# Kernel optimization log

Hardware: AMD Instinct MI355X
Metric: run time of the kernel (lower is better)

Reference implementation:

```python
import jax, jax.numpy as jnp
import numpy as np

B, CIN, COUT, H, W = 8, 256, 256, 64, 64


def setup_inputs() -> dict:
    key = jax.random.key(0)
    k1, k2, k3 = jax.random.split(key, 3)
    x = jax.random.normal(k1, (B, CIN, H, W), dtype=jnp.float32)
    style = jax.random.normal(k2, (B, CIN), dtype=jnp.float32)
    # kaiming_normal_ (fan_in = CIN*3*3, gain = sqrt(2))
    fan_in = CIN * 9
    weight = jax.random.normal(k3, (COUT, CIN, 3, 3), dtype=jnp.float32) * np.sqrt(2.0 / fan_in)
    return {"x": x, "style": style, "weight": weight}


def reference(x, style, weight):
    b, cin, h, w = x.shape
    cout = weight.shape[0]
    # modulate: [B, Cout, Cin, 3, 3]
    mw = style[:, None, :, None, None] * weight[None]
    # demodulate
    sigma = jnp.sqrt(jnp.sum(mw * mw, axis=(2, 3, 4), keepdims=True) + 1e-8)
    dw = mw / sigma
    # per-sample conv via grouped convolution (groups = B)
    x_g = x.reshape(1, b * cin, h, w)
    w_g = dw.reshape(b * cout, cin, 3, 3)
    out = jax.lax.conv_general_dilated(
        x_g, w_g,
        window_strides=(1, 1),
        padding=((1, 1), (1, 1)),
        feature_group_count=b,
        dimension_numbers=("NCHW", "OIHW", "NCHW"),
    )
    return out.reshape(b, cout, h, w)
```

## Files before the change

kernel.cpp:

```cpp
#include <hip/hip_runtime.h>

#define B_ 8
#define CIN_ 256
#define COUT_ 256

typedef short short8_t __attribute__((ext_vector_type(8)));
typedef float float4_t __attribute__((ext_vector_type(4)));

#define DWA_SHORTS   (B_ * 9 * 32 * COUT_ * 8)
#define XPRE_SHORTS  (B_ * 8 * 66 * 66 * 32)

__device__ __forceinline__ unsigned short f2bf(float f) {
    union { float f; unsigned u; } v; v.f = f;
    unsigned u = v.u;
    unsigned r = (u + 0x7fffu + ((u >> 16) & 1u)) >> 16;
    return (unsigned short)r;
}

__global__ __launch_bounds__(256) void k_xpre(const float* __restrict__ x,
                                              unsigned short* __restrict__ xpre) {
    const int h = blockIdx.x, cb = blockIdx.y, b = blockIdx.z;
    const int t = threadIdx.x;
    const int w = t >> 2, g = t & 3;
    const float* xp = x + (((size_t)(b * CIN_ + cb * 32 + g * 8)) * 64 + h) * 64 + w;
    short8_t v;
#pragma unroll
    for (int j = 0; j < 8; ++j) v[j] = (short)f2bf(xp[(size_t)j * 4096]);
    size_t dst = ((((size_t)(b * 8 + cb)) * 66 + (h + 1)) * 66 + (w + 1)) * 32 + (size_t)g * 8;
    *(short8_t*)(xpre + dst) = v;
}

__global__ __launch_bounds__(256) void k_modulate(const float* __restrict__ weight,
                                                  const float* __restrict__ style,
                                                  unsigned short* __restrict__ dwA) {
    const int b = blockIdx.y;
    const int co = blockIdx.x * 8 + (threadIdx.x & 7);
    const int oct = threadIdx.x >> 3;
    const int lane = threadIdx.x & 63, wid = threadIdx.x >> 6;

    float wreg[72];
    const float* wp = weight + (size_t)co * (CIN_ * 9) + oct * 72;
#pragma unroll
    for (int i = 0; i < 18; ++i)
        *(float4*)(wreg + 4 * i) = *(const float4*)(wp + 4 * i);

    float s[8];
#pragma unroll
    for (int j = 0; j < 8; ++j) s[j] = style[b * CIN_ + oct * 8 + j];

    float part = 0.f;
#pragma unroll
    for (int j = 0; j < 8; ++j) {
        float a = 0.f;
#pragma unroll
        for (int t9 = 0; t9 < 9; ++t9) a += wreg[j * 9 + t9] * wreg[j * 9 + t9];
        part += s[j] * s[j] * a;
    }
    part += __shfl_xor(part, 8, 64);
    part += __shfl_xor(part, 16, 64);
    part += __shfl_xor(part, 32, 64);
    __shared__ float red[4][8];
    if ((lane >> 3) == 0) red[wid][lane & 7] = part;
    __syncthreads();
    const int co_l = threadIdx.x & 7;
    const float tot = red[0][co_l] + red[1][co_l] + red[2][co_l] + red[3][co_l];
    const float inv = 1.0f / sqrtf(tot + 1e-8f);

#pragma unroll
    for (int tap = 0; tap < 9; ++tap) {
        short8_t o;
#pragma unroll
        for (int j = 0; j < 8; ++j) o[j] = (short)f2bf(wreg[j * 9 + tap] * s[j] * inv);
        size_t dst = ((((size_t)(b * 9 + tap)) * 32 + oct) * 256 + co) * 8;
        *(short8_t*)(dwA + dst) = o;
    }
}

__global__ __launch_bounds__(256) void k_conv(const unsigned short* __restrict__ xpre,
                                              const unsigned short* __restrict__ dwA,
                                              float* __restrict__ out) {
    __shared__ __align__(16) unsigned short xs[2][4 * 66 * 40];

    const int rowgrp = blockIdx.x;
    const int co_tile = blockIdx.y;
    const int b = blockIdx.z;
    const int tid = threadIdx.x;
    const int lane = tid & 63, wid = tid >> 6;
    const int wave_m = wid >> 1, wave_n = wid & 1;
    const int quad = lane >> 4, l16 = lane & 15;
    const int r0 = rowgrp * 2;
    const int co_base = co_tile * 128 + wave_m * 64;

    float4_t acc[4][4];
#pragma unroll
    for (int mi = 0; mi < 4; ++mi)
#pragma unroll
        for (int ni = 0; ni < 4; ++ni) acc[mi][ni] = (float4_t){0.f, 0.f, 0.f, 0.f};

    short8_t st[5];
    auto load_regs = [&](int cb) {
        const unsigned short* s = xpre + ((size_t)((b * 8 + cb) * 66 + r0)) * 2112;
#pragma unroll
        for (int it = 0; it < 4; ++it)
            st[it] = *(const short8_t*)(s + (size_t)(tid + it * 256) * 8);
        if (tid < 32) st[4] = *(const short8_t*)(s + (size_t)(tid + 1024) * 8);
    };
    auto store_lds = [&](int buf) {
        unsigned short* d = xs[buf];
#pragma unroll
        for (int it = 0; it < 4; ++it) {
            int c = tid + it * 256;
            *(short8_t*)(d + (c >> 2) * 40 + (c & 3) * 8) = st[it];
        }
        if (tid < 32) {
            int c = tid + 1024;
            *(short8_t*)(d + (c >> 2) * 40 + (c & 3) * 8) = st[4];
        }
    };

    load_regs(0);

    for (int cb = 0; cb < 8; ++cb) {
        short8_t aA[4], aB[4];
        {
            const unsigned short* Ab = dwA + ((size_t)(b * 9 + 0) * 32 + cb * 4 + quad) * 2048;
#pragma unroll
            for (int mi = 0; mi < 4; ++mi)
                aA[mi] = *(const short8_t*)(Ab + (co_base + mi * 16 + l16) * 8);
        }
        store_lds(cb & 1);
        __syncthreads();
        if (cb < 7) load_regs(cb + 1);

        const unsigned short* xb = xs[cb & 1];
#pragma unroll
        for (int tap = 0; tap < 9; ++tap) {
            if (tap < 8) {
                const unsigned short* Ab =
                    dwA + ((size_t)(b * 9 + tap + 1) * 32 + cb * 4 + quad) * 2048;
                short8_t* an = (tap & 1) ? aA : aB;
#pragma unroll
                for (int mi = 0; mi < 4; ++mi)
                    an[mi] = *(const short8_t*)(Ab + (co_base + mi * 16 + l16) * 8);
            }
            const int dh = tap / 3, dwc = tap % 3;
            const unsigned short* brow = xb + (wave_n + dh) * 66 * 40;
            short8_t bf[4];
#pragma unroll
            for (int ni = 0; ni < 4; ++ni)
                bf[ni] = *(const short8_t*)(brow + (ni * 16 + l16 + dwc) * 40 + quad * 8);
            const short8_t* ac = (tap & 1) ? aB : aA;
#pragma unroll
            for (int mi = 0; mi < 4; ++mi)
#pragma unroll
                for (int ni = 0; ni < 4; ++ni)
                    acc[mi][ni] = __builtin_amdgcn_mfma_f32_16x16x32_bf16(
                        ac[mi], bf[ni], acc[mi][ni], 0, 0, 0);
        }
    }

    const int orow = r0 + wave_n;
#pragma unroll
    for (int mi = 0; mi < 4; ++mi)
#pragma unroll
        for (int ni = 0; ni < 4; ++ni)
#pragma unroll
            for (int r = 0; r < 4; ++r) {
                int co = co_base + mi * 16 + quad * 4 + r;
                int c = ni * 16 + l16;
                out[(((size_t)b * COUT_ + co) * 64 + orow) * 64 + c] = acc[mi][ni][r];
            }
}

extern "C" void kernel_launch(void* const* d_in, const int* in_sizes, int n_in,
                              void* d_out, int out_size, void* d_ws, size_t ws_size,
                              hipStream_t stream) {
    const float* x = (const float*)d_in[0];
    const float* style = (const float*)d_in[1];
    const float* weight = (const float*)d_in[2];
    float* out = (float*)d_out;

    unsigned short* dwA = (unsigned short*)d_ws;
    unsigned short* xpre = dwA + DWA_SHORTS;

    hipMemsetAsync((void*)xpre, 0, (size_t)XPRE_SHORTS * 2, stream);
    k_xpre<<<dim3(64, 8, B_), 256, 0, stream>>>(x, xpre);
    k_modulate<<<dim3(32, B_), 256, 0, stream>>>(weight, style, dwA);
    k_conv<<<dim3(32, 2, B_), 256, 0, stream>>>(xpre, dwA, out);
}
```

Measured before the change: 142.6 us.

## Drop padding memset, restructure weight modulation, and deepen A-operand prefetch

The input-packing kernel now writes the zero halo itself across 66 rows, so the separate memset launch over the padded buffer is removed. The modulation kernel loads each weight slice once into LDS and handles all batch samples per block, reducing redundant weight reads, but it now writes scalar 2-byte stores. The convolution kernel keeps a 3-deep register ring of weight fragments, prefetching two taps ahead and across channel-block boundaries to hide global load latency, at the cost of more registers.

Result: no change. 141.8 us (-0.6%).

```diff
diff --git a/kernel.cpp b/kernel.cpp
--- a/kernel.cpp
+++ b/kernel.cpp
@@ -19,61 +19,82 @@
 
 __global__ __launch_bounds__(256) void k_xpre(const float* __restrict__ x,
                                               unsigned short* __restrict__ xpre) {
-    const int h = blockIdx.x, cb = blockIdx.y, b = blockIdx.z;
+    const int h_out = blockIdx.x;
+    const int cb = blockIdx.y, b = blockIdx.z;
     const int t = threadIdx.x;
-    const int w = t >> 2, g = t & 3;
-    const float* xp = x + (((size_t)(b * CIN_ + cb * 32 + g * 8)) * 64 + h) * 64 + w;
-    short8_t v;
-#pragma unroll
-    for (int j = 0; j < 8; ++j) v[j] = (short)f2bf(xp[(size_t)j * 4096]);
-    size_t dst = ((((size_t)(b * 8 + cb)) * 66 + (h + 1)) * 66 + (w + 1)) * 32 + (size_t)g * 8;
-    *(short8_t*)(xpre + dst) = v;
+    const int h_in = h_out - 1;
+    unsigned short* dst_row = xpre + (((size_t)(b * 8 + cb) * 66 + h_out)) * 66 * 32;
+#pragma unroll
+    for (int pass = 0; pass < 2; ++pass) {
+        int p = t + pass * 256;
+        if (p >= 264) break;
+        int w_out = p >> 2, g = p & 3;
+        int w_in = w_out - 1;
+        short8_t v = (short8_t){0, 0, 0, 0, 0, 0, 0, 0};
+        if ((unsigned)h_in < 64u && (unsigned)w_in < 64u) {
+            const float* xp = x + (((size_t)(b * CIN_ + cb * 32 + g * 8)) * 64 + h_in) * 64 + w_in;
+#pragma unroll
+            for (int j = 0; j < 8; ++j) v[j] = (short)f2bf(xp[(size_t)j * 4096]);
+        }
+        *(short8_t*)(dst_row + (size_t)w_out * 32 + g * 8) = v;
+    }
 }
 
 __global__ __launch_bounds__(256) void k_modulate(const float* __restrict__ weight,
                                                   const float* __restrict__ style,
                                                   unsigned short* __restrict__ dwA) {
-    const int b = blockIdx.y;
-    const int co = blockIdx.x * 8 + (threadIdx.x & 7);
-    const int oct = threadIdx.x >> 3;
-    const int lane = threadIdx.x & 63, wid = threadIdx.x >> 6;
-
-    float wreg[72];
-    const float* wp = weight + (size_t)co * (CIN_ * 9) + oct * 72;
-#pragma unroll
-    for (int i = 0; i < 18; ++i)
-        *(float4*)(wreg + 4 * i) = *(const float4*)(wp + 4 * i);
-
-    float s[8];
-#pragma unroll
-    for (int j = 0; j < 8; ++j) s[j] = style[b * CIN_ + oct * 8 + j];
-
-    float part = 0.f;
-#pragma unroll
-    for (int j = 0; j < 8; ++j) {
+    __shared__ float wlds[4 * 2304];
+    const int t = threadIdx.x;
+    const int co0 = blockIdx.x * 4;
+    const int co_l = t >> 6;
+    const int lane = t & 63;
+    const int co = co0 + co_l;
+
+    const float* wp = weight + (size_t)co0 * 2304;
+#pragma unroll
+    for (int k = 0; k < 36; ++k) wlds[t + 256 * k] = wp[t + 256 * k];
+    __syncthreads();
+
+    float wv[4][9];
+    float ss[4];
+#pragma unroll
+    for (int k = 0; k < 4; ++k) {
         float a = 0.f;
 #pragma unroll
-        for (int t9 = 0; t9 < 9; ++t9) a += wreg[j * 9 + t9] * wreg[j * 9 + t9];
-        part += s[j] * s[j] * a;
-    }
-    part += __shfl_xor(part, 8, 64);
-    part += __shfl_xor(part, 16, 64);
-    part += __shfl_xor(part, 32, 64);
-    __shared__ float red[4][8];
-    if ((lane >> 3) == 0) red[wid][lane & 7] = part;
-    __syncthreads();
-    const int co_l = threadIdx.x & 7;
-    const float tot = red[0][co_l] + red[1][co_l] + red[2][co_l] + red[3][co_l];
-    const float inv = 1.0f / sqrtf(tot + 1e-8f);
-
-#pragma unroll
-    for (int tap = 0; tap < 9; ++tap) {
-        short8_t o;
-#pragma unroll
-        for (int j = 0; j < 8; ++j) o[j] = (short)f2bf(wreg[j * 9 + tap] * s[j] * inv);
-        size_t dst = ((((size_t)(b * 9 + tap)) * 32 + oct) * 256 + co) * 8;
-        *(short8_t*)(dwA + dst) = o;
-    }
+        for (int tap = 0; tap < 9; ++tap) {
+            float w = wlds[co_l * 2304 + (lane + 64 * k) * 9 + tap];
+            wv[k][tap] = w;
+            a += w * w;
+        }
+        ss[k] = a;
+    }
+    float sv[8][4];
+#pragma unroll
+    for (int b = 0; b < 8; ++b)
+#pragma unroll
+        for (int k = 0; k < 4; ++k) sv[b][k] = style[b * CIN_ + lane + 64 * k];
+
+    float inv[8];
+#pragma unroll
+    for (int b = 0; b < 8; ++b) {
+        float part = 0.f;
+#pragma unroll
+        for (int k = 0; k < 4; ++k) part += sv[b][k] * sv[b][k] * ss[k];
+#pragma unroll
+        for (int off = 32; off > 0; off >>= 1) part += __shfl_xor(part, off, 64);
+        inv[b] = 1.0f / sqrtf(part + 1e-8f);
+    }
+
+    const size_t base = (size_t)co * 8 + (lane & 7) + (size_t)(lane >> 3) * 2048;
+#pragma unroll
+    for (int b = 0; b < 8; ++b)
+#pragma unroll
+        for (int tap = 0; tap < 9; ++tap)
+#pragma unroll
+            for (int k = 0; k < 4; ++k) {
+                size_t addr = ((size_t)(b * 9 + tap) * 32 + k * 8) * 2048 + base;
+                dwA[addr] = f2bf(wv[k][tap] * sv[b][k] * inv[b]);
+            }
 }
 
 __global__ __launch_bounds__(256) void k_conv(const unsigned short* __restrict__ xpre,
@@ -118,16 +139,19 @@
         }
     };
 
+    short8_t abuf[3][4];
+    auto loadA = [&](short8_t* dst, int acb, int atap) {
+        const unsigned short* Ab = dwA + ((size_t)(b * 9 + atap) * 32 + acb * 4 + quad) * 2048;
+#pragma unroll
+        for (int mi = 0; mi < 4; ++mi)
+            dst[mi] = *(const short8_t*)(Ab + (co_base + mi * 16 + l16) * 8);
+    };
+
     load_regs(0);
+    loadA(abuf[0], 0, 0);
+    loadA(abuf[1], 0, 1);
 
     for (int cb = 0; cb < 8; ++cb) {
-        short8_t aA[4], aB[4];
-        {
-            const unsigned short* Ab = dwA + ((size_t)(b * 9 + 0) * 32 + cb * 4 + quad) * 2048;
-#pragma unroll
-            for (int mi = 0; mi < 4; ++mi)
-                aA[mi] = *(const short8_t*)(Ab + (co_base + mi * 16 + l16) * 8);
-        }
         store_lds(cb & 1);
         __syncthreads();
         if (cb < 7) load_regs(cb + 1);
@@ -135,21 +159,18 @@
         const unsigned short* xb = xs[cb & 1];
 #pragma unroll
         for (int tap = 0; tap < 9; ++tap) {
-            if (tap < 8) {
-                const unsigned short* Ab =
-                    dwA + ((size_t)(b * 9 + tap + 1) * 32 + cb * 4 + quad) * 2048;
-                short8_t* an = (tap & 1) ? aA : aB;
-#pragma unroll
-                for (int mi = 0; mi < 4; ++mi)
-                    an[mi] = *(const short8_t*)(Ab + (co_base + mi * 16 + l16) * 8);
-            }
+            const int nl = tap + 2;
+            const int acb = cb + nl / 9, atap = nl % 9;
+            if (acb < 8) loadA(abuf[nl % 3], acb, atap);
+
             const int dh = tap / 3, dwc = tap % 3;
             const unsigned short* brow = xb + (wave_n + dh) * 66 * 40;
             short8_t bf[4];
 #pragma unroll
             for (int ni = 0; ni < 4; ++ni)
                 bf[ni] = *(const short8_t*)(brow + (ni * 16 + l16 + dwc) * 40 + quad * 8);
-            const short8_t* ac = (tap & 1) ? aB : aA;
+
+            const short8_t* ac = abuf[tap % 3];
 #pragma unroll
             for (int mi = 0; mi < 4; ++mi)
 #pragma unroll
@@ -183,8 +204,7 @@
     unsigned short* dwA = (unsigned short*)d_ws;
     unsigned short* xpre = dwA + DWA_SHORTS;
 
-    hipMemsetAsync((void*)xpre, 0, (size_t)XPRE_SHORTS * 2, stream);
-    k_xpre<<<dim3(64, 8, B_), 256, 0, stream>>>(x, xpre);
-    k_modulate<<<dim3(32, B_), 256, 0, stream>>>(weight, style, dwA);
+    k_xpre<<<dim3(66, 8, B_), 256, 0, stream>>>(x, xpre);
+    k_modulate<<<dim3(64), 256, 0, stream>>>(weight, style, dwA);
     k_conv<<<dim3(32, 2, B_), 256, 0, stream>>>(xpre, dwA, out);
 }
```
